# Kernel optimization log

Hardware: AMD Instinct MI355X
Metric: run time of the kernel (lower is better)

Reference implementation:

```python
import jax, jax.numpy as jnp
import numpy as np

B, C, N = 8, 64, 4096
C_OUT = 64
K = 20
EPS = 1e-5
NEG_SLOPE = 0.2


def setup_inputs() -> dict:
    key = jax.random.key(0)
    k1, k2 = jax.random.split(key)
    x = jax.random.normal(k1, (B, C, N), dtype=jnp.float32)
    # Conv2d(2C, C_out, 1, bias=False) weight, squeezed to (C_out, 2C)
    W = jax.random.normal(k2, (C_OUT, 2 * C), dtype=jnp.float32) * (1.0 / np.sqrt(2 * C))
    gamma = jnp.ones((C_OUT,), dtype=jnp.float32)
    beta = jnp.zeros((C_OUT,), dtype=jnp.float32)
    return {"x": x, "W": W, "gamma": gamma, "beta": beta}


def reference(x, W, gamma, beta):
    # x: (B, C, N)
    x_t = jnp.swapaxes(x, 1, 2)                      # (B, N, C)
    xx = jnp.sum(x_t * x_t, axis=2, keepdims=True)   # (B, N, 1)
    # pairwise_dist = -||xi||^2 + 2 xi.xj - ||xj||^2  (negative squared dist)
    pairwise = 2.0 * jnp.einsum('bnc,bmc->bnm', x_t, x_t) - xx - jnp.swapaxes(xx, 1, 2)
    _, idx = jax.lax.top_k(pairwise, K)              # (B, N, K) nearest neighbors

    # gather neighbor features: neighbors[b,c,n,j] = x[b,c,idx[b,n,j]]
    neighbors = jax.vmap(lambda xb, ib: xb[:, ib])(x, idx)   # (B, C, N, K)
    x_exp = x[:, :, :, None]                                 # (B, C, N, 1)
    edge = jnp.concatenate(
        [jnp.broadcast_to(x_exp, neighbors.shape), neighbors - x_exp], axis=1
    )                                                        # (B, 2C, N, K)

    # 1x1 conv (no bias)
    h = jnp.einsum('oc,bcnk->bonk', W, edge)                 # (B, C_out, N, K)

    # BatchNorm2d (training mode: batch statistics over B, N, K)
    mean = jnp.mean(h, axis=(0, 2, 3), keepdims=True)
    var = jnp.var(h, axis=(0, 2, 3), keepdims=True)
    hn = (h - mean) * jax.lax.rsqrt(var + EPS)
    hn = hn * gamma[None, :, None, None] + beta[None, :, None, None]

    # LeakyReLU(0.2) then max over k
    act = jnp.where(hn >= 0, hn, NEG_SLOPE * hn)
    return jnp.max(act, axis=-1)                             # (B, C_out, N)
```

## Files before the change

### kernel.cpp

```cpp
#include <hip/hip_runtime.h>
#include <hip/hip_bf16.h>
#include <math.h>

#define BB 8
#define CC 64
#define NN 4096
#define CO 64
#define KK 20
#define BN (BB*NN)
#define CN (CC*NN)
#define EPSV 1e-5
#define NEG_SLOPE 0.2f
#define CNT_TOTAL 655360.0
#define CAP 64
#define MARGIN 0.75f

typedef unsigned short U16;
typedef unsigned int u32;
typedef unsigned long long u64;
typedef __attribute__((ext_vector_type(8))) __bf16 bf16x8;
typedef __attribute__((ext_vector_type(16))) float f32x16;

#define OFF_P1    ((size_t)0)
#define OFF_P2    ((size_t)8388608)
#define OFF_XX    ((size_t)16777216)
#define OFF_IDX   ((size_t)16908288)
#define OFF_XT    ((size_t)19529728)
#define OFF_XB    ((size_t)27918336)
#define OFF_TV    ((size_t)36306944)
#define OFF_THR   ((size_t)57278464)
#define OFF_CAND  ((size_t)57409536)
#define OFF_CCNT  ((size_t)65798144)
#define OFF_SUMS  ((size_t)65929216)
#define OFF_MAXH  ((size_t)36306944)
#define OFF_MINH  ((size_t)44695552)

#define NET_INS(dv) { const float d_ = (dv); _Pragma("unroll") \
  for (int q_ = KK-1; q_ >= 1; --q_) tv[q_] = __builtin_amdgcn_fmed3f(tv[q_-1], d_, tv[q_]); \
  tv[0] = fmaxf(tv[0], d_); }

__global__ __launch_bounds__(256) void k0_repack(
    const float* __restrict__ x, float* __restrict__ XT,
    U16* __restrict__ XB) {
  __shared__ float tile[64*65];
  const int b = blockIdx.y, n0 = blockIdx.x*64, t = threadIdx.x;
#pragma unroll
  for (int r = 0; r < 16; ++r) {
    const int c = r*4 + (t>>6);
    const int nn = t & 63;
    tile[c*65 + nn] = x[(size_t)b*CN + (size_t)c*NN + n0 + nn];
  }
  __syncthreads();
  const int g = t>>6, pos = t&63;
  float v[16];
#pragma unroll
  for (int cc = 0; cc < 16; ++cc) v[cc] = tile[(g*16+cc)*65 + pos];
  const size_t base = ((size_t)(b*NN + n0 + pos))*64 + g*16;
#pragma unroll
  for (int u = 0; u < 4; ++u)
    *(float4*)(XT + base + u*4) = make_float4(v[u*4],v[u*4+1],v[u*4+2],v[u*4+3]);
  U16 hb[16];
#pragma unroll
  for (int cc = 0; cc < 16; ++cc) {
    __hip_bfloat16 h = __float2bfloat16(v[cc]);
    hb[cc] = reinterpret_cast<U16&>(h);
  }
  uint hw[8];
#pragma unroll
  for (int u = 0; u < 8; ++u) hw[u] = (uint)hb[2*u] | ((uint)hb[2*u+1] << 16);
  *(uint4*)(XB + base)     = make_uint4(hw[0],hw[1],hw[2],hw[3]);
  *(uint4*)(XB + base + 8) = make_uint4(hw[4],hw[5],hw[6],hw[7]);
}

__global__ __launch_bounds__(256) void k1_project(
    const float* __restrict__ x, const float* __restrict__ W,
    float* __restrict__ p1, float* __restrict__ p2, float* __restrict__ xx) {
  __shared__ float Wt[64*128];
  __shared__ float xt[64*64];
  const int b  = blockIdx.y;
  const int n0 = blockIdx.x * 64;
  const int t  = threadIdx.x;

#pragma unroll
  for (int r = 0; r < 16; ++r) {
    const int lin = r*256 + t;
    const int c = lin >> 6, o = lin & 63;
    const float w1 = W[o*128 + c];
    const float w2 = W[o*128 + 64 + c];
    Wt[c*128 + o]      = w1 - w2;
    Wt[c*128 + 64 + o] = w2;
  }
#pragma unroll
  for (int r = 0; r < 16; ++r) {
    const int lin = r*256 + t;
    const int c = lin >> 6, pt = lin & 63;
    xt[c*64 + pt] = x[((size_t)b*64 + c)*NN + n0 + pt];
  }
  __syncthreads();

  const int o0  = (t & 31) * 4;
  const int pt0 = (t >> 5) * 8;
  float acc[4][8];
#pragma unroll
  for (int i = 0; i < 4; ++i)
#pragma unroll
    for (int j = 0; j < 8; ++j) acc[i][j] = 0.f;

  for (int c = 0; c < 64; ++c) {
    const float4 w4 = *(const float4*)(Wt + c*128 + o0);
    const float4 xa = *(const float4*)(xt + c*64 + pt0);
    const float4 xb = *(const float4*)(xt + c*64 + pt0 + 4);
    float wv[4] = {w4.x, w4.y, w4.z, w4.w};
    float xv[8] = {xa.x, xa.y, xa.z, xa.w, xb.x, xb.y, xb.z, xb.w};
#pragma unroll
    for (int i = 0; i < 4; ++i)
#pragma unroll
      for (int j = 0; j < 8; ++j) acc[i][j] = fmaf(wv[i], xv[j], acc[i][j]);
  }

  float* basep = (o0 < 64) ? (p1 + o0) : (p2 + o0 - 64);
#pragma unroll
  for (int j = 0; j < 8; ++j) {
    const size_t pn = (size_t)b*NN + n0 + pt0 + j;
    *(float4*)(basep + pn*64) = make_float4(acc[0][j], acc[1][j], acc[2][j], acc[3][j]);
  }

  if (t < 64) {
    float s = 0.f;
    for (int c = 0; c < 64; ++c) s = fmaf(xt[c*64 + t], xt[c*64 + t], s);
    xx[b*NN + n0 + t] = s;
  }
}

#define LOADA(ch, A0_,A1_,A2_,A3_) { \
  const U16* ap_ = XB + (bnn + jbase + (size_t)(ch)*32 + lo5)*64 + ch0; \
  A0_ = *(const bf16x8*)(ap_);      A1_ = *(const bf16x8*)(ap_+16); \
  A2_ = *(const bf16x8*)(ap_+32);   A3_ = *(const bf16x8*)(ap_+48); }

#define DOCHUNK(ch, A0_,A1_,A2_,A3_) { \
  f32x16 acc_; \
  _Pragma("unroll") for (int r_ = 0; r_ < 16; ++r_) acc_[r_] = 0.f; \
  acc_ = __builtin_amdgcn_mfma_f32_32x32x16_bf16(A0_, Bi0, acc_, 0,0,0); \
  acc_ = __builtin_amdgcn_mfma_f32_32x32x16_bf16(A1_, Bi1, acc_, 0,0,0); \
  acc_ = __builtin_amdgcn_mfma_f32_32x32x16_bf16(A2_, Bi2, acc_, 0,0,0); \
  acc_ = __builtin_amdgcn_mfma_f32_32x32x16_bf16(A3_, Bi3, acc_, 0,0,0); \
  const float* xp_ = xxs + (ch)*32 + 4*hi5; \
  const float4 x0_ = *(const float4*)(xp_); \
  const float4 x1_ = *(const float4*)(xp_ + 8); \
  const float4 x2_ = *(const float4*)(xp_ + 16); \
  const float4 x3_ = *(const float4*)(xp_ + 24); \
  float xa_[16]; \
  xa_[0]=x0_.x; xa_[1]=x0_.y; xa_[2]=x0_.z; xa_[3]=x0_.w; \
  xa_[4]=x1_.x; xa_[5]=x1_.y; xa_[6]=x1_.z; xa_[7]=x1_.w; \
  xa_[8]=x2_.x; xa_[9]=x2_.y; xa_[10]=x2_.z; xa_[11]=x2_.w; \
  xa_[12]=x3_.x; xa_[13]=x3_.y; xa_[14]=x3_.z; xa_[15]=x3_.w; \
  if constexpr (MODE == 0) { \
    _Pragma("unroll") for (int r_ = 0; r_ < 16; ++r_) \
      NET_INS(fmaf(2.f, acc_[r_], -xa_[r_])) \
  } else { \
    const int jb_ = jbase + (ch)*32 + 4*hi5; \
    _Pragma("unroll") for (int r_ = 0; r_ < 16; ++r_) { \
      const float dd_ = fmaf(2.f, acc_[r_], -xa_[r_]); \
      if (dd_ >= thrv) { \
        const int pos_ = atomicAdd(&ccnt[rowg], 1); \
        if (pos_ < CAP) cand[rowg*CAP + pos_] = jb_ + (r_&3) + 8*(r_>>2); \
      } \
    } \
  } }

template<int MODE>
__global__ __launch_bounds__(256, 4) void k2ab(
    const U16* __restrict__ XB, const float* __restrict__ xx,
    float* __restrict__ TV, const float* __restrict__ thr,
    int* __restrict__ ccnt, int* __restrict__ cand) {
  __shared__ float xxs[1024];
  const int L = blockIdx.x;
  const int b = L & 7, q = (L >> 3) & 3, bx = L >> 5;
  const int i0 = bx * 128;
  const int t = threadIdx.x, w = t>>6, l = t&63, lo5 = l&31, hi5 = l>>5;
  const int ch0 = 8*hi5;
  const size_t bnn = (size_t)b*NN;
  const int jbase = q*1024;
  const size_t rowg = bnn + i0 + w*32 + lo5;

  *(float4*)(xxs + t*4) = *(const float4*)(xx + bnn + jbase + t*4);
  __syncthreads();

  const U16* bp = XB + rowg*64 + ch0;
  const bf16x8 Bi0 = *(const bf16x8*)(bp);
  const bf16x8 Bi1 = *(const bf16x8*)(bp + 16);
  const bf16x8 Bi2 = *(const bf16x8*)(bp + 32);
  const bf16x8 Bi3 = *(const bf16x8*)(bp + 48);

  float tv[KK];
  float thrv = 0.f;
  if constexpr (MODE == 0) {
#pragma unroll
    for (int k = 0; k < KK; ++k) tv[k] = -INFINITY;
  } else {
    thrv = thr[rowg];
  }

  bf16x8 AE0,AE1,AE2,AE3, AO0,AO1,AO2,AO3;
  LOADA(0, AE0,AE1,AE2,AE3)
  for (int c2 = 0; c2 < 16; ++c2) {
    LOADA(2*c2+1, AO0,AO1,AO2,AO3)
    DOCHUNK(2*c2, AE0,AE1,AE2,AE3)
    if (c2 < 15) LOADA(2*c2+2, AE0,AE1,AE2,AE3)
    DOCHUNK(2*c2+1, AO0,AO1,AO2,AO3)
  }

  if constexpr (MODE == 0) {
    const int part = q*2 + hi5;
#pragma unroll
    for (int k = 0; k < KK; ++k) TV[(size_t)(part*KK + k)*BN + rowg] = tv[k];
  }
}

__global__ __launch_bounds__(256) void k2b_thr(
    const float* __restrict__ TV, float* __restrict__ thr) {
  const int rowg = blockIdx.x*256 + threadIdx.x;
  float tv[KK];
#pragma unroll
  for (int k = 0; k < KK; ++k) tv[k] = -INFINITY;
  for (int u = 0; u < 8*KK; ++u) NET_INS(TV[(size_t)u*BN + rowg])
  thr[rowg] = tv[KK-1] - MARGIN;
}

__global__ __launch_bounds__(256) void k2e_exact(
    const float* __restrict__ XT, const float* __restrict__ xx,
    const int* __restrict__ ccnt, const int* __restrict__ cand,
    int* __restrict__ idxo) {
  const int t = threadIdx.x, w = t>>6, l = t&63;
  const int L = blockIdx.x;
  const int bbase = (L & 7) * NN;
  const int rowg = bbase + (L >> 3)*64 + w*16 + (l>>2);
  const int g = l & 3;
  const float* xip = XT + (size_t)rowg*64 + g*16;
  const float4 xi0 = *(const float4*)(xip),   xi1 = *(const float4*)(xip+4);
  const float4 xi2 = *(const float4*)(xip+8), xi3 = *(const float4*)(xip+12);
  const float xxi = xx[rowg];
  const int Cr = min(ccnt[rowg], CAP);
  int cmax = Cr;
#pragma unroll
  for (int off = 1; off < 64; off <<= 1) cmax = max(cmax, __shfl_xor(cmax, off));
  u64 kv[KK];
#pragma unroll
  for (int k = 0; k < KK; ++k) kv[k] = 0ULL;

  for (int c = 0; c < cmax; ++c) {
    const bool valid = (c < Cr);
    const int jj = valid ? cand[(size_t)rowg*CAP + c] : 0;
    const float* xjp = XT + ((size_t)(bbase + jj))*64 + g*16;
    const float4 a  = *(const float4*)(xjp),   b4 = *(const float4*)(xjp+4);
    const float4 c4 = *(const float4*)(xjp+8), d4 = *(const float4*)(xjp+12);
    float p = xi0.x*a.x;
    p = fmaf(xi0.y, a.y, p);  p = fmaf(xi0.z, a.z, p);  p = fmaf(xi0.w, a.w, p);
    p = fmaf(xi1.x, b4.x, p); p = fmaf(xi1.y, b4.y, p); p = fmaf(xi1.z, b4.z, p); p = fmaf(xi1.w, b4.w, p);
    p = fmaf(xi2.x, c4.x, p); p = fmaf(xi2.y, c4.y, p); p = fmaf(xi2.z, c4.z, p); p = fmaf(xi2.w, c4.w, p);
    p = fmaf(xi3.x, d4.x, p); p = fmaf(xi3.y, d4.y, p); p = fmaf(xi3.z, d4.z, p); p = fmaf(xi3.w, d4.w, p);
    p += __shfl_xor(p, 1);
    p += __shfl_xor(p, 2);
    const float d = 2.f*p - xxi - xx[bbase + jj];
    const u32 s = __float_as_uint(d);
    const u32 k32 = (s & 0x80000000u) ? ~s : (s | 0x80000000u);
    u64 key = ((u64)k32 << 32) | (u64)(0xFFFFFFFFu - (u32)jj);
    if (!valid) key = 0ULL;
#pragma unroll
    for (int qq = KK-1; qq >= 1; --qq) {
      const u64 mn = (kv[qq-1] < key) ? kv[qq-1] : key;
      if (kv[qq] < mn) kv[qq] = mn;
    }
    if (kv[0] < key) kv[0] = key;
  }
  if (g == 0) {
#pragma unroll
    for (int k = 0; k < KK; ++k)
      idxo[(size_t)rowg*KK + k] = (int)(0xFFFFFFFFu - (u32)(kv[k] & 0xFFFFFFFFu));
  }
}

__global__ __launch_bounds__(256) void k3_gather(
    const float* __restrict__ p1, const float* __restrict__ p2,
    const int* __restrict__ idx, float* __restrict__ maxh,
    float* __restrict__ minh, double* __restrict__ sums) {
  const int t = threadIdx.x;
  const int g = t >> 6, o = t & 63;
  const int L = blockIdx.x;
  const int bbase = (L & 7) * NN;
  const int pn0 = bbase + (L >> 3)*64 + g*16;
  float sacc = 0.f, ssacc = 0.f;

  for (int p = 0; p < 16; ++p) {
    const int pn = pn0 + p;
    const float p1v = p1[(size_t)pn*64 + o];
    const int* ip = idx + (size_t)pn*KK;
    float mx = -INFINITY, mn = INFINITY;
#pragma unroll
    for (int k = 0; k < KK; ++k) {
      const int j = ip[k];
      const float p2v = p2[((size_t)(bbase + j))*64 + o];
      const float h = p1v + p2v;
      mx = fmaxf(mx, h); mn = fminf(mn, h);
      sacc += h; ssacc += h*h;
    }
    maxh[(size_t)pn*64 + o] = mx;
    minh[(size_t)pn*64 + o] = mn;
  }

  __shared__ float rs[256], rss[256];
  rs[t] = sacc; rss[t] = ssacc;
  __syncthreads();
  if (t < 64) {
    const double sv  = (double)rs[t]  + (double)rs[t+64]  + (double)rs[t+128]  + (double)rs[t+192];
    const double ssv = (double)rss[t] + (double)rss[t+64] + (double)rss[t+128] + (double)rss[t+192];
    atomicAdd(&sums[t], sv);
    atomicAdd(&sums[64 + t], ssv);
  }
}

__global__ __launch_bounds__(256) void k4_out(
    const float* __restrict__ maxh, const float* __restrict__ minh,
    const double* __restrict__ sums, const float* __restrict__ gamma,
    const float* __restrict__ beta, float* __restrict__ out) {
  __shared__ float sc_[64], sh_[64];
  __shared__ float lmax[64*65], lmin[64*65];
  const int b  = blockIdx.y;
  const int n0 = blockIdx.x * 64;
  const int t  = threadIdx.x;

  if (t < 64) {
    const double mean = sums[t] / CNT_TOTAL;
    const double var  = sums[64 + t] / CNT_TOTAL - mean*mean;
    const float scale = gamma[t] * (float)(1.0 / sqrt(var + EPSV));
    sc_[t] = scale;
    sh_[t] = beta[t] - (float)mean * scale;
  }
#pragma unroll
  for (int r = 0; r < 16; ++r) {
    const int linear = r*256 + t;
    const int o = linear & 63, pos = linear >> 6;
    const size_t gg = ((size_t)(b*NN) + n0 + pos)*64 + o;
    lmax[o*65 + pos] = maxh[gg];
    lmin[o*65 + pos] = minh[gg];
  }
  __syncthreads();

  const int nn = t & 63;
  const int obase = (t >> 6) * 16;
#pragma unroll
  for (int r = 0; r < 16; ++r) {
    const int o = obase + r;
    const float scale = sc_[o], shift = sh_[o];
    const float src = (scale >= 0.f) ? lmax[o*65 + nn] : lmin[o*65 + nn];
    float v = scale*src + shift;
    v = (v >= 0.f) ? v : NEG_SLOPE*v;
    out[(size_t)b*CO*NN + (size_t)o*NN + n0 + nn] = v;
  }
}

extern "C" void kernel_launch(void* const* d_in, const int* in_sizes, int n_in,
                              void* d_out, int out_size, void* d_ws, size_t ws_size,
                              hipStream_t stream) {
  const float* x     = (const float*)d_in[0];
  const float* W     = (const float*)d_in[1];
  const float* gamma = (const float*)d_in[2];
  const float* beta  = (const float*)d_in[3];
  float* out = (float*)d_out;
  char* ws = (char*)d_ws;

  float*  p1   = (float*)(ws + OFF_P1);
  float*  p2   = (float*)(ws + OFF_P2);
  float*  xx   = (float*)(ws + OFF_XX);
  int*    idx  = (int*)  (ws + OFF_IDX);
  float*  XT   = (float*)(ws + OFF_XT);
  U16*    XB   = (U16*)  (ws + OFF_XB);
  float*  TV   = (float*)(ws + OFF_TV);
  float*  thr  = (float*)(ws + OFF_THR);
  int*    cand = (int*)  (ws + OFF_CAND);
  int*    ccnt = (int*)  (ws + OFF_CCNT);
  float*  maxh = (float*)(ws + OFF_MAXH);
  float*  minh = (float*)(ws + OFF_MINH);
  double* sums = (double*)(ws + OFF_SUMS);

  hipMemsetAsync(ws + OFF_CCNT, 0, (OFF_SUMS - OFF_CCNT) + 1024, stream);

  k0_repack <<<dim3(NN/64, BB), 256, 0, stream>>>(x, XT, XB);
  k1_project<<<dim3(NN/64, BB), 256, 0, stream>>>(x, W, p1, p2, xx);
  k2ab<0>   <<<dim3(1024), 256, 0, stream>>>(XB, xx, TV, thr, ccnt, cand);
  k2b_thr   <<<dim3(BN/256), 256, 0, stream>>>(TV, thr);
  k2ab<1>   <<<dim3(1024), 256, 0, stream>>>(XB, xx, TV, thr, ccnt, cand);
  k2e_exact <<<dim3(BN/64), 256, 0, stream>>>(XT, xx, ccnt, cand, idx);
  k3_gather <<<dim3(BN/64), 256, 0, stream>>>(p1, p2, idx, maxh, minh, sums);
  k4_out    <<<dim3(NN/64, BB), 256, 0, stream>>>(maxh, minh, sums, gamma, beta, out);
}
```

Measured before the change: 355.0 us.

## Use MFMA-fragment bf16 layout, split kNN scan finer, store partial top-k as bf16

```diff
diff --git a/kernel.cpp b/kernel.cpp
--- a/kernel.cpp
+++ b/kernel.cpp
@@ -13,7 +13,7 @@
 #define NEG_SLOPE 0.2f
 #define CNT_TOTAL 655360.0
 #define CAP 64
-#define MARGIN 0.75f
+#define MARGIN 3.0f
 
 typedef unsigned short U16;
 typedef unsigned int u32;
@@ -26,7 +26,7 @@
 #define OFF_XX    ((size_t)16777216)
 #define OFF_IDX   ((size_t)16908288)
 #define OFF_XT    ((size_t)19529728)
-#define OFF_XB    ((size_t)27918336)
+#define OFF_XBF   ((size_t)27918336)
 #define OFF_TV    ((size_t)36306944)
 #define OFF_THR   ((size_t)57278464)
 #define OFF_CAND  ((size_t)57409536)
@@ -41,7 +41,7 @@
 
 __global__ __launch_bounds__(256) void k0_repack(
     const float* __restrict__ x, float* __restrict__ XT,
-    U16* __restrict__ XB) {
+    U16* __restrict__ XBF) {
   __shared__ float tile[64*65];
   const int b = blockIdx.y, n0 = blockIdx.x*64, t = threadIdx.x;
 #pragma unroll
@@ -68,8 +68,10 @@
   uint hw[8];
 #pragma unroll
   for (int u = 0; u < 8; ++u) hw[u] = (uint)hb[2*u] | ((uint)hb[2*u+1] << 16);
-  *(uint4*)(XB + base)     = make_uint4(hw[0],hw[1],hw[2],hw[3]);
-  *(uint4*)(XB + base + 8) = make_uint4(hw[4],hw[5],hw[6],hw[7]);
+  const size_t rb = (size_t)(b*NN + n0 + pos) >> 5;
+  U16* xo = XBF + rb*2048 + (size_t)g*512 + (size_t)(pos & 31)*8;
+  *(uint4*)(xo)       = make_uint4(hw[0],hw[1],hw[2],hw[3]);
+  *(uint4*)(xo + 256) = make_uint4(hw[4],hw[5],hw[6],hw[7]);
 }
 
 __global__ __launch_bounds__(256) void k1_project(
@@ -133,9 +135,9 @@
 }
 
 #define LOADA(ch, A0_,A1_,A2_,A3_) { \
-  const U16* ap_ = XB + (bnn + jbase + (size_t)(ch)*32 + lo5)*64 + ch0; \
-  A0_ = *(const bf16x8*)(ap_);      A1_ = *(const bf16x8*)(ap_+16); \
-  A2_ = *(const bf16x8*)(ap_+32);   A3_ = *(const bf16x8*)(ap_+48); }
+  const U16* ap_ = XBF + (size_t)(bnn + jbase + (ch)*32)*64 + (size_t)l*8; \
+  A0_ = *(const bf16x8*)(ap_);        A1_ = *(const bf16x8*)(ap_+512); \
+  A2_ = *(const bf16x8*)(ap_+1024);   A3_ = *(const bf16x8*)(ap_+1536); }
 
 #define DOCHUNK(ch, A0_,A1_,A2_,A3_) { \
   f32x16 acc_; \
@@ -169,28 +171,27 @@
   } }
 
 template<int MODE>
-__global__ __launch_bounds__(256, 4) void k2ab(
-    const U16* __restrict__ XB, const float* __restrict__ xx,
-    float* __restrict__ TV, const float* __restrict__ thr,
+__global__ __launch_bounds__(256, 3) void k2ab(
+    const U16* __restrict__ XBF, const float* __restrict__ xx,
+    U16* __restrict__ TVb, const float* __restrict__ thr,
     int* __restrict__ ccnt, int* __restrict__ cand) {
-  __shared__ float xxs[1024];
+  __shared__ float xxs[512];
   const int L = blockIdx.x;
-  const int b = L & 7, q = (L >> 3) & 3, bx = L >> 5;
+  const int b = L & 7, q = (L >> 3) & 7, bx = L >> 6;
   const int i0 = bx * 128;
   const int t = threadIdx.x, w = t>>6, l = t&63, lo5 = l&31, hi5 = l>>5;
-  const int ch0 = 8*hi5;
   const size_t bnn = (size_t)b*NN;
-  const int jbase = q*1024;
+  const int jbase = q*512;
   const size_t rowg = bnn + i0 + w*32 + lo5;
 
-  *(float4*)(xxs + t*4) = *(const float4*)(xx + bnn + jbase + t*4);
+  if (t < 128) *(float4*)(xxs + t*4) = *(const float4*)(xx + bnn + jbase + t*4);
   __syncthreads();
 
-  const U16* bp = XB + rowg*64 + ch0;
+  const U16* bp = XBF + (size_t)(rowg >> 5)*2048 + (size_t)hi5*256 + (size_t)(rowg & 31)*8;
   const bf16x8 Bi0 = *(const bf16x8*)(bp);
-  const bf16x8 Bi1 = *(const bf16x8*)(bp + 16);
-  const bf16x8 Bi2 = *(const bf16x8*)(bp + 32);
-  const bf16x8 Bi3 = *(const bf16x8*)(bp + 48);
+  const bf16x8 Bi1 = *(const bf16x8*)(bp + 512);
+  const bf16x8 Bi2 = *(const bf16x8*)(bp + 1024);
+  const bf16x8 Bi3 = *(const bf16x8*)(bp + 1536);
 
   float tv[KK];
   float thrv = 0.f;
@@ -203,27 +204,33 @@
 
   bf16x8 AE0,AE1,AE2,AE3, AO0,AO1,AO2,AO3;
   LOADA(0, AE0,AE1,AE2,AE3)
-  for (int c2 = 0; c2 < 16; ++c2) {
+  for (int c2 = 0; c2 < 8; ++c2) {
     LOADA(2*c2+1, AO0,AO1,AO2,AO3)
     DOCHUNK(2*c2, AE0,AE1,AE2,AE3)
-    if (c2 < 15) LOADA(2*c2+2, AE0,AE1,AE2,AE3)
+    if (c2 < 7) LOADA(2*c2+2, AE0,AE1,AE2,AE3)
     DOCHUNK(2*c2+1, AO0,AO1,AO2,AO3)
   }
 
   if constexpr (MODE == 0) {
     const int part = q*2 + hi5;
 #pragma unroll
-    for (int k = 0; k < KK; ++k) TV[(size_t)(part*KK + k)*BN + rowg] = tv[k];
+    for (int k = 0; k < KK; ++k) {
+      __hip_bfloat16 h = __float2bfloat16(tv[k]);
+      TVb[(size_t)(part*KK + k)*BN + rowg] = reinterpret_cast<U16&>(h);
+    }
   }
 }
 
 __global__ __launch_bounds__(256) void k2b_thr(
-    const float* __restrict__ TV, float* __restrict__ thr) {
+    const U16* __restrict__ TVb, float* __restrict__ thr) {
   const int rowg = blockIdx.x*256 + threadIdx.x;
   float tv[KK];
 #pragma unroll
   for (int k = 0; k < KK; ++k) tv[k] = -INFINITY;
-  for (int u = 0; u < 8*KK; ++u) NET_INS(TV[(size_t)u*BN + rowg])
+  for (int u = 0; u < 16*KK; ++u) {
+    const float d = __uint_as_float((u32)TVb[(size_t)u*BN + rowg] << 16);
+    NET_INS(d)
+  }
   thr[rowg] = tv[KK-1] - MARGIN;
 }
 
@@ -374,8 +381,8 @@
   float*  xx   = (float*)(ws + OFF_XX);
   int*    idx  = (int*)  (ws + OFF_IDX);
   float*  XT   = (float*)(ws + OFF_XT);
-  U16*    XB   = (U16*)  (ws + OFF_XB);
-  float*  TV   = (float*)(ws + OFF_TV);
+  U16*    XBF  = (U16*)  (ws + OFF_XBF);
+  U16*    TVb  = (U16*)  (ws + OFF_TV);
   float*  thr  = (float*)(ws + OFF_THR);
   int*    cand = (int*)  (ws + OFF_CAND);
   int*    ccnt = (int*)  (ws + OFF_CCNT);
@@ -385,11 +392,11 @@
 
   hipMemsetAsync(ws + OFF_CCNT, 0, (OFF_SUMS - OFF_CCNT) + 1024, stream);
 
-  k0_repack <<<dim3(NN/64, BB), 256, 0, stream>>>(x, XT, XB);
+  k0_repack <<<dim3(NN/64, BB), 256, 0, stream>>>(x, XT, XBF);
   k1_project<<<dim3(NN/64, BB), 256, 0, stream>>>(x, W, p1, p2, xx);
-  k2ab<0>   <<<dim3(1024), 256, 0, stream>>>(XB, xx, TV, thr, ccnt, cand);
-  k2b_thr   <<<dim3(BN/256), 256, 0, stream>>>(TV, thr);
-  k2ab<1>   <<<dim3(1024), 256, 0, stream>>>(XB, xx, TV, thr, ccnt, cand);
+  k2ab<0>   <<<dim3(2048), 256, 0, stream>>>(XBF, xx, TVb, thr, ccnt, cand);
+  k2b_thr   <<<dim3(BN/256), 256, 0, stream>>>(TVb, thr);
+  k2ab<1>   <<<dim3(2048), 256, 0, stream>>>(XBF, xx, TVb, thr, ccnt, cand);
   k2e_exact <<<dim3(BN/64), 256, 0, stream>>>(XT, xx, ccnt, cand, idx);
   k3_gather <<<dim3(BN/64), 256, 0, stream>>>(p1, p2, idx, maxh, minh, sums);
   k4_out    <<<dim3(NN/64, BB), 256, 0, stream>>>(maxh, minh, sums, gamma, beta, out);
```

Measured after the change: 378.2 us. 6.5% more time.
